# Kernel optimization log

Hardware: AMD Instinct MI355X
Metric: run time of the kernel (lower is better)

Reference implementation:

```python
import math
import jax, jax.numpy as jnp
import numpy as np

N_STEPS = 4
D_ENERGY = 128
FEATURE_DIM = 1024
B, N = 4, 2048


def setup_inputs() -> dict:
    key = jax.random.key(0)
    ks = jax.random.split(key, 5)
    scale = 1.0 / math.sqrt(FEATURE_DIM)
    return {
        "features": jax.random.normal(ks[0], (B, N, FEATURE_DIM), dtype=jnp.float32),
        "W_q": jax.random.normal(ks[1], (FEATURE_DIM, D_ENERGY), dtype=jnp.float32) * scale,
        "W_k": jax.random.normal(ks[2], (FEATURE_DIM, D_ENERGY), dtype=jnp.float32) * scale,
        "charge_w": jax.random.normal(ks[3], (FEATURE_DIM, 1), dtype=jnp.float32) * scale,
        "charge_b": jnp.zeros((1,), dtype=jnp.float32),
        "locality_scale": jnp.float32(1.0),
        "step_size": jnp.float32(0.5),
        "charge_decay": jnp.float32(0.3),
    }


def reference(features, W_q, W_k, charge_w, charge_b, locality_scale, step_size, charge_decay):
    Bn, Nn, _ = features.shape
    # compatibility: [B,N,N]
    Q = jnp.einsum("bnf,fe->bne", features, W_q)
    K = jnp.einsum("bnf,fe->bne", features, W_k)
    compat = jnp.einsum("bqe,bke->bqk", Q, K) / jnp.sqrt(jnp.float32(D_ENERGY))
    # locality bias: locality_scale / max(|i-j|, 1)
    pos = jnp.arange(Nn, dtype=jnp.float32)
    dist = jnp.maximum(jnp.abs(pos[None, :] - pos[:, None]), 1.0)
    locality = locality_scale / dist  # [N,N]
    # initial charge in (0,1): [B,N]
    charge = jax.nn.sigmoid(jnp.einsum("bnf,fo->bno", features, charge_w)[..., 0] + charge_b[0])
    base = compat + locality[None]  # [B,N,N], fixed across steps
    logits = base
    for _ in range(N_STEPS):
        attn = jax.nn.softmax(logits, axis=-1)
        received = attn.sum(axis=-2)  # [B,N] column sums
        charge = charge * (1.0 - charge_decay * jax.nn.sigmoid(received - 1.0))
        energy = -base * charge[..., :, None] * charge[..., None, :]
        logits = logits - step_size * energy
    return jax.nn.softmax(logits, axis=-1)
```

## Files before the change

### kernel.cpp

```cpp
#include <hip/hip_runtime.h>
#include <math.h>

namespace {
constexpr int NB = 4;
constexpr int NN = 2048;
constexpr int FD = 1024;
constexpr int DE = 128;
constexpr int BN = NB * NN;

constexpr size_t PARTQ_OFF = 0;
constexpr size_t PARTK_OFF = 4194304;
constexpr size_t FH_OFF    = 8388608;
constexpr size_t FL_OFF    = 12582912;
constexpr size_t QKHL_OFF  = 16777216;
constexpr size_t C_OFF     = QKHL_OFF + 2097152;
}

typedef __attribute__((ext_vector_type(8))) short bf16x8;
typedef __attribute__((ext_vector_type(4))) float f32x4;
typedef __attribute__((ext_vector_type(4))) _Float16 f16x4;

__device__ __forceinline__ unsigned short bf16_hi(float x) {
    unsigned u = __float_as_uint(x);
    unsigned r = (u + 0x7fffu + ((u >> 16) & 1u)) >> 16;
    return (unsigned short)r;
}
__device__ __forceinline__ float bf16_val(unsigned short h) {
    return __uint_as_float((unsigned)h << 16);
}


__global__ __launch_bounds__(256) void convert_F(
        const float* __restrict__ feat, unsigned short* __restrict__ Fh,
        unsigned short* __restrict__ Fl) {
    const int g = blockIdx.x * 256 + threadIdx.x;
    const int tile = g >> 6, lane = g & 63;
    const int tr = tile >> 5, fc = tile & 31;
    const int row = tr * 16 + (lane & 15);
    const int f0 = fc * 32 + (lane >> 4) * 8;
    const float* src = &feat[(size_t)row * FD + f0];
    ushort4 h0, l0, h1, l1;
    float4 a = *(const float4*)src;
    float4 b = *(const float4*)(src + 4);
    h0.x = bf16_hi(a.x); l0.x = bf16_hi(a.x - bf16_val(h0.x));
    h0.y = bf16_hi(a.y); l0.y = bf16_hi(a.y - bf16_val(h0.y));
    h0.z = bf16_hi(a.z); l0.z = bf16_hi(a.z - bf16_val(h0.z));
    h0.w = bf16_hi(a.w); l0.w = bf16_hi(a.w - bf16_val(h0.w));
    h1.x = bf16_hi(b.x); l1.x = bf16_hi(b.x - bf16_val(h1.x));
    h1.y = bf16_hi(b.y); l1.y = bf16_hi(b.y - bf16_val(h1.y));
    h1.z = bf16_hi(b.z); l1.z = bf16_hi(b.z - bf16_val(h1.z));
    h1.w = bf16_hi(b.w); l1.w = bf16_hi(b.w - bf16_val(h1.w));
    const size_t dst = (size_t)tile * 512 + lane * 8;
    *(ushort4*)&Fh[dst] = h0; *(ushort4*)&Fh[dst + 4] = h1;
    *(ushort4*)&Fl[dst] = l0; *(ushort4*)&Fl[dst + 4] = l1;
}

__global__ __launch_bounds__(256) void convert_W(
        const float* __restrict__ Wq, const float* __restrict__ Wk,
        unsigned short* __restrict__ Wqh, unsigned short* __restrict__ Wql,
        unsigned short* __restrict__ Wkh, unsigned short* __restrict__ Wkl) {
    const int g = blockIdx.x * 256 + threadIdx.x;
    const int tile = g >> 6, lane = g & 63;
    const int ec = tile >> 5, fc = tile & 31;
    const int e = ec * 16 + (lane & 15);
    const int f0 = fc * 32 + (lane >> 4) * 8;
    const float* W = blockIdx.y ? Wk : Wq;
    unsigned short* Th = blockIdx.y ? Wkh : Wqh;
    unsigned short* Tl = blockIdx.y ? Wkl : Wql;
    unsigned short hh[8], ll[8];
    #pragma unroll
    for (int j = 0; j < 8; ++j) {
        float v = W[(size_t)(f0 + j) * DE + e];
        hh[j] = bf16_hi(v); ll[j] = bf16_hi(v - bf16_val(hh[j]));
    }
    const size_t dst = (size_t)tile * 512 + lane * 8;
    *(ushort4*)&Th[dst]     = make_ushort4(hh[0], hh[1], hh[2], hh[3]);
    *(ushort4*)&Th[dst + 4] = make_ushort4(hh[4], hh[5], hh[6], hh[7]);
    *(ushort4*)&Tl[dst]     = make_ushort4(ll[0], ll[1], ll[2], ll[3]);
    *(ushort4*)&Tl[dst + 4] = make_ushort4(ll[4], ll[5], ll[6], ll[7]);
}

__global__ __launch_bounds__(256) void charge_init(
        const float* __restrict__ feat, const float* __restrict__ cw,
        const float* __restrict__ cb, float* __restrict__ c0) {
    const int wave = threadIdx.x >> 6, lane = threadIdx.x & 63;
    const int r = blockIdx.x * 4 + wave;
    const float* fr = feat + (size_t)r * FD;
    float s = 0.f;
    #pragma unroll
    for (int k = 0; k < 16; ++k) { int f = lane + 64 * k; s += fr[f] * cw[f]; }
    for (int off = 32; off > 0; off >>= 1) s += __shfl_xor(s, off);
    if (lane == 0) {
        float x = s + cb[0];
        c0[r] = 1.f / (1.f + __expf(-x));
    }
}

__global__ __launch_bounds__(256) void qk_mfma(
        const unsigned short* __restrict__ Fh, const unsigned short* __restrict__ Fl,
        const unsigned short* __restrict__ Wqh, const unsigned short* __restrict__ Wql,
        const unsigned short* __restrict__ Wkh, const unsigned short* __restrict__ Wkl,
        float* __restrict__ partQ, float* __restrict__ partK) {
    const int tid = threadIdx.x;
    const int w = tid >> 6, lane = tid & 63;
    const int quad = lane >> 4, l16 = lane & 15;
    const int kc = blockIdx.x;
    const int tr0 = blockIdx.y * 4;
    const unsigned short* Bh = (w < 2) ? Wqh : Wkh;
    const unsigned short* Bl = (w < 2) ? Wql : Wkl;
    const int ec0 = (w & 1) * 4;
    float* part = ((w < 2) ? partQ : partK) + (size_t)kc * BN * DE;

    f32x4 acc[4][4];
    #pragma unroll
    for (int a = 0; a < 4; ++a)
        #pragma unroll
        for (int c = 0; c < 4; ++c) acc[a][c] = (f32x4){0.f, 0.f, 0.f, 0.f};

    #pragma unroll 2
    for (int ch = 0; ch < 8; ++ch) {
        const int fc = kc * 8 + ch;
        bf16x8 aH[4], aL[4];
        #pragma unroll
        for (int rt = 0; rt < 4; ++rt) {
            const size_t off = ((size_t)((tr0 + rt) * 32 + fc) * 64 + lane) * 8;
            aH[rt] = *(const bf16x8*)&Fh[off];
            aL[rt] = *(const bf16x8*)&Fl[off];
        }
        #pragma unroll
        for (int ct = 0; ct < 4; ++ct) {
            const size_t off = ((size_t)((ec0 + ct) * 32 + fc) * 64 + lane) * 8;
            bf16x8 bH = *(const bf16x8*)&Bh[off];
            bf16x8 bL = *(const bf16x8*)&Bl[off];
            #pragma unroll
            for (int rt = 0; rt < 4; ++rt) {
                acc[rt][ct] = __builtin_amdgcn_mfma_f32_16x16x32_bf16(aH[rt], bH, acc[rt][ct], 0, 0, 0);
                acc[rt][ct] = __builtin_amdgcn_mfma_f32_16x16x32_bf16(aH[rt], bL, acc[rt][ct], 0, 0, 0);
                acc[rt][ct] = __builtin_amdgcn_mfma_f32_16x16x32_bf16(aL[rt], bH, acc[rt][ct], 0, 0, 0);
            }
        }
    }
    #pragma unroll
    for (int rt = 0; rt < 4; ++rt)
        #pragma unroll
        for (int ct = 0; ct < 4; ++ct)
            #pragma unroll
            for (int reg = 0; reg < 4; ++reg) {
                const int row = (tr0 + rt) * 16 + quad * 4 + reg;
                const int e = (ec0 + ct) * 16 + l16;
                part[(size_t)row * DE + e] = acc[rt][ct][reg];
            }
}

__global__ __launch_bounds__(256) void qk_reduce(
        const float* __restrict__ partQ, const float* __restrict__ partK,
        unsigned short* __restrict__ Qh, unsigned short* __restrict__ Ql,
        unsigned short* __restrict__ Kh, unsigned short* __restrict__ Kl) {
    const size_t i4 = ((size_t)blockIdx.x * 256 + threadIdx.x) * 4;
    float4 q = {0.f, 0.f, 0.f, 0.f}, k = {0.f, 0.f, 0.f, 0.f};
    #pragma unroll
    for (int c = 0; c < 4; ++c) {
        float4 a = *(const float4*)&partQ[(size_t)c * BN * DE + i4];
        float4 b = *(const float4*)&partK[(size_t)c * BN * DE + i4];
        q.x += a.x; q.y += a.y; q.z += a.z; q.w += a.w;
        k.x += b.x; k.y += b.y; k.z += b.z; k.w += b.w;
    }
    const int row = (int)(i4 >> 7);
    const int k0  = (int)(i4 & 127);
    const int kc = k0 >> 5, quad = (k0 >> 3) & 3, j = k0 & 7;
    const int lane = quad * 16 + (row & 15);
    const size_t dst = ((size_t)((row >> 4) * 4 + kc) * 64 + lane) * 8 + j;
    ushort4 h, l;
    h.x = bf16_hi(q.x); l.x = bf16_hi(q.x - bf16_val(h.x));
    h.y = bf16_hi(q.y); l.y = bf16_hi(q.y - bf16_val(h.y));
    h.z = bf16_hi(q.z); l.z = bf16_hi(q.z - bf16_val(h.z));
    h.w = bf16_hi(q.w); l.w = bf16_hi(q.w - bf16_val(h.w));
    *(ushort4*)&Qh[dst] = h; *(ushort4*)&Ql[dst] = l;
    h.x = bf16_hi(k.x); l.x = bf16_hi(k.x - bf16_val(h.x));
    h.y = bf16_hi(k.y); l.y = bf16_hi(k.y - bf16_val(h.y));
    h.z = bf16_hi(k.z); l.z = bf16_hi(k.z - bf16_val(h.z));
    h.w = bf16_hi(k.w); l.w = bf16_hi(k.w - bf16_val(h.w));
    *(ushort4*)&Kh[dst] = h; *(ushort4*)&Kl[dst] = l;
}

__global__ __launch_bounds__(256) void base_mfma(
        const unsigned short* __restrict__ Qh, const unsigned short* __restrict__ Ql,
        const unsigned short* __restrict__ Kh, const unsigned short* __restrict__ Kl,
        const float* __restrict__ d_ls, _Float16* __restrict__ baseH) {
    const int tid = threadIdx.x;
    const int w = tid >> 6, lane = tid & 63;
    const int quad = lane >> 4, l16 = lane & 15;
    const int b = blockIdx.z;
    const int i0 = blockIdx.y * 128, j0 = blockIdx.x * 128;
    const int trA0 = (b * NN + i0) / 16 + w * 2;
    const int trB0 = (b * NN + j0) / 16;

    f32x4 acc[2][8];
    #pragma unroll
    for (int a = 0; a < 2; ++a)
        #pragma unroll
        for (int c = 0; c < 8; ++c) acc[a][c] = (f32x4){0.f, 0.f, 0.f, 0.f};

    #pragma unroll
    for (int kc = 0; kc < 4; ++kc) {
        bf16x8 aH[2], aL[2];
        #pragma unroll
        for (int rt = 0; rt < 2; ++rt) {
            const size_t off = ((size_t)((trA0 + rt) * 4 + kc) * 64 + lane) * 8;
            aH[rt] = *(const bf16x8*)&Qh[off];
            aL[rt] = *(const bf16x8*)&Ql[off];
        }
        #pragma unroll
        for (int ct = 0; ct < 8; ++ct) {
            const size_t off = ((size_t)((trB0 + ct) * 4 + kc) * 64 + lane) * 8;
            bf16x8 bH = *(const bf16x8*)&Kh[off];
            bf16x8 bL = *(const bf16x8*)&Kl[off];
            #pragma unroll
            for (int rt = 0; rt < 2; ++rt) {
                acc[rt][ct] = __builtin_amdgcn_mfma_f32_16x16x32_bf16(aH[rt], bH, acc[rt][ct], 0, 0, 0);
                acc[rt][ct] = __builtin_amdgcn_mfma_f32_16x16x32_bf16(aH[rt], bL, acc[rt][ct], 0, 0, 0);
                acc[rt][ct] = __builtin_amdgcn_mfma_f32_16x16x32_bf16(aL[rt], bH, acc[rt][ct], 0, 0, 0);
            }
        }
    }
    const float ls = d_ls[0];
    const float rs = 0.08838834764831845f;
    #pragma unroll
    for (int rt = 0; rt < 2; ++rt)
        #pragma unroll
        for (int reg = 0; reg < 4; ++reg) {
            const int i = i0 + w * 32 + rt * 16 + quad * 4 + reg;
            _Float16* brow = baseH + ((size_t)b * NN + i) * NN;
            #pragma unroll
            for (int ct = 0; ct < 8; ++ct) {
                const int j = j0 + ct * 16 + l16;
                const float dist = fmaxf(fabsf((float)(i - j)), 1.0f);
                brow[j] = (_Float16)(acc[rt][ct][reg] * rs + ls / dist);
            }
        }
}

template <int T>
__device__ __forceinline__ void row_core(
        const f16x4 (&hv)[8], const float* __restrict__ chg1,
        const float (&ci)[T > 0 ? T : 1], const int lane,
        float (&x)[32], float& inv) {
    float mx = -1e30f;
    #pragma unroll
    for (int k = 0; k < 8; ++k) {
        const int c = k * 256 + lane * 4;
        float m0 = 1.f, m1 = 1.f, m2 = 1.f, m3 = 1.f;
        #pragma unroll
        for (int u = 0; u < T; ++u) {
            const float4 cj = *(const float4*)&chg1[(size_t)u * BN + c];
            m0 += ci[u] * cj.x; m1 += ci[u] * cj.y;
            m2 += ci[u] * cj.z; m3 += ci[u] * cj.w;
        }
        x[k * 4 + 0] = (float)hv[k][0] * m0;
        x[k * 4 + 1] = (float)hv[k][1] * m1;
        x[k * 4 + 2] = (float)hv[k][2] * m2;
        x[k * 4 + 3] = (float)hv[k][3] * m3;
        mx = fmaxf(mx, fmaxf(fmaxf(x[k * 4], x[k * 4 + 1]),
                             fmaxf(x[k * 4 + 2], x[k * 4 + 3])));
    }
    #pragma unroll
    for (int off = 32; off > 0; off >>= 1) mx = fmaxf(mx, __shfl_xor(mx, off));
    float se = 0.f;
    #pragma unroll
    for (int q = 0; q < 32; ++q) { x[q] = __expf(x[q] - mx); se += x[q]; }
    #pragma unroll
    for (int off = 32; off > 0; off >>= 1) se += __shfl_xor(se, off);
    inv = 1.f / se;
}

template <int T, bool WO>
__global__ __launch_bounds__(256) void step_pass(
        const _Float16* __restrict__ base, const float* __restrict__ charge,
        const float* __restrict__ d_ss, float* __restrict__ P,
        float* __restrict__ out) {
    constexpr int CS_W = WO ? 1 : 4;
    constexpr int CS_N = WO ? 1 : NN;
    __shared__ float colsum[CS_W][CS_N];
    const int tid = threadIdx.x;
    const int w = tid >> 6, lane = tid & 63;
    const int blk = blockIdx.x;
    const int b = blk >> 8;
    const int r0 = (blk & 255) * 8;
    const float ss = d_ss[0];
    const size_t cb = (size_t)b << 11;
    const size_t ri0 = cb + r0 + w * 2;
    const _Float16* row0 = base + ri0 * NN;
    const _Float16* row1 = row0 + NN;
    const float* chg1 = charge + (size_t)BN + cb;

    f16x4 hv0[8], hv1[8];
    #pragma unroll
    for (int k = 0; k < 8; ++k) {
        const int c = k * 256 + lane * 4;
        hv0[k] = *(const f16x4*)&row0[c];
        hv1[k] = *(const f16x4*)&row1[c];
    }
    float ci0[T > 0 ? T : 1], ci1[T > 0 ? T : 1];
    #pragma unroll
    for (int u = 0; u < T; ++u) {
        ci0[u] = charge[(size_t)(u + 1) * BN + ri0] * ss;
        ci1[u] = charge[(size_t)(u + 1) * BN + ri0 + 1] * ss;
    }

    float col_acc[32];
    if (!WO) {
        #pragma unroll
        for (int q = 0; q < 32; ++q) col_acc[q] = 0.f;
    }

    float x[32]; float inv;
    row_core<T>(hv0, chg1, ci0, lane, x, inv);
    if (WO) {
        #pragma unroll
        for (int k = 0; k < 8; ++k) {
            const int c = k * 256 + lane * 4;
            float4 o = {x[k * 4 + 0] * inv, x[k * 4 + 1] * inv,
                        x[k * 4 + 2] * inv, x[k * 4 + 3] * inv};
            *(float4*)&out[ri0 * NN + c] = o;
        }
    } else {
        #pragma unroll
        for (int q = 0; q < 32; ++q) col_acc[q] += x[q] * inv;
    }
    row_core<T>(hv1, chg1, ci1, lane, x, inv);
    if (WO) {
        #pragma unroll
        for (int k = 0; k < 8; ++k) {
            const int c = k * 256 + lane * 4;
            float4 o = {x[k * 4 + 0] * inv, x[k * 4 + 1] * inv,
                        x[k * 4 + 2] * inv, x[k * 4 + 3] * inv};
            *(float4*)&out[(ri0 + 1) * NN + c] = o;
        }
    } else {
        #pragma unroll
        for (int q = 0; q < 32; ++q) col_acc[q] += x[q] * inv;
    }

    if (!WO) {
        #pragma unroll
        for (int k = 0; k < 8; ++k)
            *(float4*)&colsum[w][k * 256 + lane * 4] = *(float4*)&col_acc[k * 4];
        __syncthreads();
        float* prow = P + (size_t)blk * NN;
        #pragma unroll
        for (int k = 0; k < 8; ++k) {
            const int c = tid + 256 * k;
            prow[c] = colsum[0][c] + colsum[1][c] + colsum[2][c] + colsum[3][c];
        }
    }
}

__global__ __launch_bounds__(256) void charge_reduce(
        const float* __restrict__ P, const float* __restrict__ d_decay,
        const float* __restrict__ c_prev, float* __restrict__ c_next) {
    const int b = blockIdx.x >> 3;
    const int col = ((blockIdx.x & 7) << 8) + threadIdx.x;
    const float* p = P + ((size_t)b * 256) * NN + col;
    float s = 0.f;
    #pragma unroll 8
    for (int r = 0; r < 256; ++r) s += p[(size_t)r * NN];
    const int gi = (b << 11) + col;
    const float sg = 1.f / (1.f + __expf(1.f - s));
    c_next[gi] = c_prev[gi] * (1.f - d_decay[0] * sg);
}

extern "C" void kernel_launch(void* const* d_in, const int* in_sizes, int n_in,
                              void* d_out, int out_size, void* d_ws, size_t ws_size,
                              hipStream_t stream) {
    const float* feat  = (const float*)d_in[0];
    const float* Wq    = (const float*)d_in[1];
    const float* Wk    = (const float*)d_in[2];
    const float* cw    = (const float*)d_in[3];
    const float* cb    = (const float*)d_in[4];
    const float* ls    = (const float*)d_in[5];
    const float* ssp   = (const float*)d_in[6];
    const float* decay = (const float*)d_in[7];

    float* ws   = (float*)d_ws;
    float* partQ = ws + PARTQ_OFF;
    float* partK = ws + PARTK_OFF;
    unsigned short* Fh = (unsigned short*)(ws + FH_OFF);
    unsigned short* Fl = (unsigned short*)(ws + FL_OFF);
    unsigned short* qkhl = (unsigned short*)(ws + QKHL_OFF);
    unsigned short* Qh = qkhl;
    unsigned short* Ql = qkhl + (size_t)BN * DE;
    unsigned short* Kh = qkhl + (size_t)2 * BN * DE;
    unsigned short* Kl = qkhl + (size_t)3 * BN * DE;
    unsigned short* Wqh = qkhl;
    unsigned short* Wql = qkhl + (size_t)DE * FD;
    unsigned short* Wkh = qkhl + (size_t)2 * DE * FD;
    unsigned short* Wkl = qkhl + (size_t)3 * DE * FD;
    float* charge = ws + C_OFF;
    _Float16* baseH = (_Float16*)(ws + PARTQ_OFF);
    float* P      = ws + FH_OFF;
    float* out    = (float*)d_out;

    convert_F<<<BN * FD / 8 / 256, 256, 0, stream>>>(feat, Fh, Fl);
    convert_W<<<dim3(64, 2), 256, 0, stream>>>(Wq, Wk, Wqh, Wql, Wkh, Wkl);
    charge_init<<<BN / 4, 256, 0, stream>>>(feat, cw, cb, charge);
    qk_mfma<<<dim3(4, BN / 64), 256, 0, stream>>>(Fh, Fl, Wqh, Wql, Wkh, Wkl, partQ, partK);
    qk_reduce<<<BN * DE / 4 / 256, 256, 0, stream>>>(partQ, partK, Qh, Ql, Kh, Kl);
    base_mfma<<<dim3(NN / 128, NN / 128, NB), 256, 0, stream>>>(Qh, Ql, Kh, Kl, ls, baseH);

    step_pass<0, false><<<1024, 256, 0, stream>>>(baseH, charge, ssp, P, nullptr);
    charge_reduce<<<32, 256, 0, stream>>>(P, decay, charge, charge + (size_t)BN);
    step_pass<1, false><<<1024, 256, 0, stream>>>(baseH, charge, ssp, P, nullptr);
    charge_reduce<<<32, 256, 0, stream>>>(P, decay, charge + (size_t)BN, charge + (size_t)2 * BN);
    step_pass<2, false><<<1024, 256, 0, stream>>>(baseH, charge, ssp, P, nullptr);
    charge_reduce<<<32, 256, 0, stream>>>(P, decay, charge + (size_t)2 * BN, charge + (size_t)3 * BN);
    step_pass<3, false><<<1024, 256, 0, stream>>>(baseH, charge, ssp, P, nullptr);
    charge_reduce<<<32, 256, 0, stream>>>(P, decay, charge + (size_t)3 * BN, charge + (size_t)4 * BN);
    step_pass<4, true><<<1024, 256, 0, stream>>>(baseH, charge, ssp, nullptr, out);
}
```

Before: 276.4 us.

## Fuse prep kernels, drop split-K QK reduce, stage charges in LDS for softmax steps

Merges the feature/weight conversion and charge-init kernels into one launch, and replaces the split-K QK projection plus reduction with a single kernel that writes hi/lo bf16 Q/K via LDS. The step passes now cache charge vectors in shared memory, use wider f16 loads, skip the softmax max subtraction, and reduce column sums in two stages. This cuts launches, partial-sum traffic and redundant global loads, at the cost of fewer blocks in the projection and reliance on bounded logits to avoid exp overflow.

```diff
diff --git a/kernel.cpp b/kernel.cpp
--- a/kernel.cpp
+++ b/kernel.cpp
@@ -8,8 +8,7 @@
 constexpr int DE = 128;
 constexpr int BN = NB * NN;
 
-constexpr size_t PARTQ_OFF = 0;
-constexpr size_t PARTK_OFF = 4194304;
+constexpr size_t WSW_OFF   = 0;
 constexpr size_t FH_OFF    = 8388608;
 constexpr size_t FL_OFF    = 12582912;
 constexpr size_t QKHL_OFF  = 16777216;
@@ -18,7 +17,7 @@
 
 typedef __attribute__((ext_vector_type(8))) short bf16x8;
 typedef __attribute__((ext_vector_type(4))) float f32x4;
-typedef __attribute__((ext_vector_type(4))) _Float16 f16x4;
+typedef __attribute__((ext_vector_type(8))) _Float16 f16x8;
 
 __device__ __forceinline__ unsigned short bf16_hi(float x) {
     unsigned u = __float_as_uint(x);
@@ -30,157 +29,132 @@
 }
 
 
-__global__ __launch_bounds__(256) void convert_F(
-        const float* __restrict__ feat, unsigned short* __restrict__ Fh,
-        unsigned short* __restrict__ Fl) {
-    const int g = blockIdx.x * 256 + threadIdx.x;
-    const int tile = g >> 6, lane = g & 63;
-    const int tr = tile >> 5, fc = tile & 31;
-    const int row = tr * 16 + (lane & 15);
-    const int f0 = fc * 32 + (lane >> 4) * 8;
-    const float* src = &feat[(size_t)row * FD + f0];
-    ushort4 h0, l0, h1, l1;
-    float4 a = *(const float4*)src;
-    float4 b = *(const float4*)(src + 4);
-    h0.x = bf16_hi(a.x); l0.x = bf16_hi(a.x - bf16_val(h0.x));
-    h0.y = bf16_hi(a.y); l0.y = bf16_hi(a.y - bf16_val(h0.y));
-    h0.z = bf16_hi(a.z); l0.z = bf16_hi(a.z - bf16_val(h0.z));
-    h0.w = bf16_hi(a.w); l0.w = bf16_hi(a.w - bf16_val(h0.w));
-    h1.x = bf16_hi(b.x); l1.x = bf16_hi(b.x - bf16_val(h1.x));
-    h1.y = bf16_hi(b.y); l1.y = bf16_hi(b.y - bf16_val(h1.y));
-    h1.z = bf16_hi(b.z); l1.z = bf16_hi(b.z - bf16_val(h1.z));
-    h1.w = bf16_hi(b.w); l1.w = bf16_hi(b.w - bf16_val(h1.w));
-    const size_t dst = (size_t)tile * 512 + lane * 8;
-    *(ushort4*)&Fh[dst] = h0; *(ushort4*)&Fh[dst + 4] = h1;
-    *(ushort4*)&Fl[dst] = l0; *(ushort4*)&Fl[dst + 4] = l1;
-}
-
-__global__ __launch_bounds__(256) void convert_W(
-        const float* __restrict__ Wq, const float* __restrict__ Wk,
+__global__ __launch_bounds__(256) void prep(
+        const float* __restrict__ feat, const float* __restrict__ Wq,
+        const float* __restrict__ Wk, const float* __restrict__ cw,
+        const float* __restrict__ cbias,
+        unsigned short* __restrict__ Fh, unsigned short* __restrict__ Fl,
         unsigned short* __restrict__ Wqh, unsigned short* __restrict__ Wql,
-        unsigned short* __restrict__ Wkh, unsigned short* __restrict__ Wkl) {
-    const int g = blockIdx.x * 256 + threadIdx.x;
-    const int tile = g >> 6, lane = g & 63;
-    const int ec = tile >> 5, fc = tile & 31;
-    const int e = ec * 16 + (lane & 15);
-    const int f0 = fc * 32 + (lane >> 4) * 8;
-    const float* W = blockIdx.y ? Wk : Wq;
-    unsigned short* Th = blockIdx.y ? Wkh : Wqh;
-    unsigned short* Tl = blockIdx.y ? Wkl : Wql;
-    unsigned short hh[8], ll[8];
-    #pragma unroll
-    for (int j = 0; j < 8; ++j) {
-        float v = W[(size_t)(f0 + j) * DE + e];
-        hh[j] = bf16_hi(v); ll[j] = bf16_hi(v - bf16_val(hh[j]));
-    }
-    const size_t dst = (size_t)tile * 512 + lane * 8;
-    *(ushort4*)&Th[dst]     = make_ushort4(hh[0], hh[1], hh[2], hh[3]);
-    *(ushort4*)&Th[dst + 4] = make_ushort4(hh[4], hh[5], hh[6], hh[7]);
-    *(ushort4*)&Tl[dst]     = make_ushort4(ll[0], ll[1], ll[2], ll[3]);
-    *(ushort4*)&Tl[dst + 4] = make_ushort4(ll[4], ll[5], ll[6], ll[7]);
-}
-
-__global__ __launch_bounds__(256) void charge_init(
-        const float* __restrict__ feat, const float* __restrict__ cw,
-        const float* __restrict__ cb, float* __restrict__ c0) {
-    const int wave = threadIdx.x >> 6, lane = threadIdx.x & 63;
-    const int r = blockIdx.x * 4 + wave;
-    const float* fr = feat + (size_t)r * FD;
-    float s = 0.f;
-    #pragma unroll
-    for (int k = 0; k < 16; ++k) { int f = lane + 64 * k; s += fr[f] * cw[f]; }
-    for (int off = 32; off > 0; off >>= 1) s += __shfl_xor(s, off);
-    if (lane == 0) {
-        float x = s + cb[0];
-        c0[r] = 1.f / (1.f + __expf(-x));
-    }
-}
-
-__global__ __launch_bounds__(256) void qk_mfma(
+        unsigned short* __restrict__ Wkh, unsigned short* __restrict__ Wkl,
+        float* __restrict__ c0) {
+    const int bid = blockIdx.x;
+    const int tid = threadIdx.x;
+    if (bid < 4096) {
+        const int g = bid * 256 + tid;
+        const int tile = g >> 6, lane = g & 63;
+        const int tr = tile >> 5, fc = tile & 31;
+        const int row = tr * 16 + (lane & 15);
+        const int f0 = fc * 32 + (lane >> 4) * 8;
+        const float* src = &feat[(size_t)row * FD + f0];
+        ushort4 h0, l0, h1, l1;
+        float4 a = *(const float4*)src;
+        float4 b = *(const float4*)(src + 4);
+        h0.x = bf16_hi(a.x); l0.x = bf16_hi(a.x - bf16_val(h0.x));
+        h0.y = bf16_hi(a.y); l0.y = bf16_hi(a.y - bf16_val(h0.y));
+        h0.z = bf16_hi(a.z); l0.z = bf16_hi(a.z - bf16_val(h0.z));
+        h0.w = bf16_hi(a.w); l0.w = bf16_hi(a.w - bf16_val(h0.w));
+        h1.x = bf16_hi(b.x); l1.x = bf16_hi(b.x - bf16_val(h1.x));
+        h1.y = bf16_hi(b.y); l1.y = bf16_hi(b.y - bf16_val(h1.y));
+        h1.z = bf16_hi(b.z); l1.z = bf16_hi(b.z - bf16_val(h1.z));
+        h1.w = bf16_hi(b.w); l1.w = bf16_hi(b.w - bf16_val(h1.w));
+        const size_t dst = (size_t)tile * 512 + lane * 8;
+        *(ushort4*)&Fh[dst] = h0; *(ushort4*)&Fh[dst + 4] = h1;
+        *(ushort4*)&Fl[dst] = l0; *(ushort4*)&Fl[dst + 4] = l1;
+    } else if (bid < 4224) {
+        const int wbid = bid - 4096;
+        const int mat = wbid >> 6;
+        const int g = (wbid & 63) * 256 + tid;
+        const int tile = g >> 6, lane = g & 63;
+        const int ec = tile >> 5, fc = tile & 31;
+        const int e = ec * 16 + (lane & 15);
+        const int f0 = fc * 32 + (lane >> 4) * 8;
+        const float* W = mat ? Wk : Wq;
+        unsigned short* Th = mat ? Wkh : Wqh;
+        unsigned short* Tl = mat ? Wkl : Wql;
+        unsigned short hh[8], ll[8];
+        #pragma unroll
+        for (int j = 0; j < 8; ++j) {
+            float v = W[(size_t)(f0 + j) * DE + e];
+            hh[j] = bf16_hi(v); ll[j] = bf16_hi(v - bf16_val(hh[j]));
+        }
+        const size_t dst = (size_t)tile * 512 + lane * 8;
+        *(ushort4*)&Th[dst]     = make_ushort4(hh[0], hh[1], hh[2], hh[3]);
+        *(ushort4*)&Th[dst + 4] = make_ushort4(hh[4], hh[5], hh[6], hh[7]);
+        *(ushort4*)&Tl[dst]     = make_ushort4(ll[0], ll[1], ll[2], ll[3]);
+        *(ushort4*)&Tl[dst + 4] = make_ushort4(ll[4], ll[5], ll[6], ll[7]);
+    } else {
+        const int wave = tid >> 6, lane = tid & 63;
+        const int r = (bid - 4224) * 4 + wave;
+        const float* fr = feat + (size_t)r * FD;
+        float s = 0.f;
+        #pragma unroll
+        for (int k = 0; k < 16; ++k) { int f = lane + 64 * k; s += fr[f] * cw[f]; }
+        for (int off = 32; off > 0; off >>= 1) s += __shfl_xor(s, off);
+        if (lane == 0) {
+            float x = s + cbias[0];
+            c0[r] = 1.f / (1.f + __expf(-x));
+        }
+    }
+}
+
+__global__ __launch_bounds__(256) void qk_proj(
         const unsigned short* __restrict__ Fh, const unsigned short* __restrict__ Fl,
         const unsigned short* __restrict__ Wqh, const unsigned short* __restrict__ Wql,
         const unsigned short* __restrict__ Wkh, const unsigned short* __restrict__ Wkl,
-        float* __restrict__ partQ, float* __restrict__ partK) {
+        unsigned short* __restrict__ Qh, unsigned short* __restrict__ Ql,
+        unsigned short* __restrict__ Kh, unsigned short* __restrict__ Kl) {
+    __shared__ unsigned short lds[8192];
     const int tid = threadIdx.x;
     const int w = tid >> 6, lane = tid & 63;
     const int quad = lane >> 4, l16 = lane & 15;
-    const int kc = blockIdx.x;
-    const int tr0 = blockIdx.y * 4;
-    const unsigned short* Bh = (w < 2) ? Wqh : Wkh;
-    const unsigned short* Bl = (w < 2) ? Wql : Wkl;
-    const int ec0 = (w & 1) * 4;
-    float* part = ((w < 2) ? partQ : partK) + (size_t)kc * BN * DE;
-
-    f32x4 acc[4][4];
-    #pragma unroll
-    for (int a = 0; a < 4; ++a)
-        #pragma unroll
-        for (int c = 0; c < 4; ++c) acc[a][c] = (f32x4){0.f, 0.f, 0.f, 0.f};
-
-    #pragma unroll 2
-    for (int ch = 0; ch < 8; ++ch) {
-        const int fc = kc * 8 + ch;
-        bf16x8 aH[4], aL[4];
-        #pragma unroll
-        for (int rt = 0; rt < 4; ++rt) {
-            const size_t off = ((size_t)((tr0 + rt) * 32 + fc) * 64 + lane) * 8;
-            aH[rt] = *(const bf16x8*)&Fh[off];
-            aL[rt] = *(const bf16x8*)&Fl[off];
-        }
+    const int blk = blockIdx.x;
+    const int mat = w >> 1, ec0 = (w & 1) * 4;
+    const unsigned short* Bh = mat ? Wkh : Wqh;
+    const unsigned short* Bl = mat ? Wkl : Wql;
+
+    f32x4 acc[4];
+    #pragma unroll
+    for (int c = 0; c < 4; ++c) acc[c] = (f32x4){0.f, 0.f, 0.f, 0.f};
+
+    for (int fc = 0; fc < 32; ++fc) {
+        const size_t aoff = ((size_t)(blk * 32 + fc) * 64 + lane) * 8;
+        bf16x8 aH = *(const bf16x8*)&Fh[aoff];
+        bf16x8 aL = *(const bf16x8*)&Fl[aoff];
         #pragma unroll
         for (int ct = 0; ct < 4; ++ct) {
-            const size_t off = ((size_t)((ec0 + ct) * 32 + fc) * 64 + lane) * 8;
-            bf16x8 bH = *(const bf16x8*)&Bh[off];
-            bf16x8 bL = *(const bf16x8*)&Bl[off];
-            #pragma unroll
-            for (int rt = 0; rt < 4; ++rt) {
-                acc[rt][ct] = __builtin_amdgcn_mfma_f32_16x16x32_bf16(aH[rt], bH, acc[rt][ct], 0, 0, 0);
-                acc[rt][ct] = __builtin_amdgcn_mfma_f32_16x16x32_bf16(aH[rt], bL, acc[rt][ct], 0, 0, 0);
-                acc[rt][ct] = __builtin_amdgcn_mfma_f32_16x16x32_bf16(aL[rt], bH, acc[rt][ct], 0, 0, 0);
-            }
-        }
-    }
-    #pragma unroll
-    for (int rt = 0; rt < 4; ++rt)
-        #pragma unroll
-        for (int ct = 0; ct < 4; ++ct)
-            #pragma unroll
-            for (int reg = 0; reg < 4; ++reg) {
-                const int row = (tr0 + rt) * 16 + quad * 4 + reg;
-                const int e = (ec0 + ct) * 16 + l16;
-                part[(size_t)row * DE + e] = acc[rt][ct][reg];
-            }
-}
-
-__global__ __launch_bounds__(256) void qk_reduce(
-        const float* __restrict__ partQ, const float* __restrict__ partK,
-        unsigned short* __restrict__ Qh, unsigned short* __restrict__ Ql,
-        unsigned short* __restrict__ Kh, unsigned short* __restrict__ Kl) {
-    const size_t i4 = ((size_t)blockIdx.x * 256 + threadIdx.x) * 4;
-    float4 q = {0.f, 0.f, 0.f, 0.f}, k = {0.f, 0.f, 0.f, 0.f};
-    #pragma unroll
-    for (int c = 0; c < 4; ++c) {
-        float4 a = *(const float4*)&partQ[(size_t)c * BN * DE + i4];
-        float4 b = *(const float4*)&partK[(size_t)c * BN * DE + i4];
-        q.x += a.x; q.y += a.y; q.z += a.z; q.w += a.w;
-        k.x += b.x; k.y += b.y; k.z += b.z; k.w += b.w;
-    }
-    const int row = (int)(i4 >> 7);
-    const int k0  = (int)(i4 & 127);
-    const int kc = k0 >> 5, quad = (k0 >> 3) & 3, j = k0 & 7;
-    const int lane = quad * 16 + (row & 15);
-    const size_t dst = ((size_t)((row >> 4) * 4 + kc) * 64 + lane) * 8 + j;
-    ushort4 h, l;
-    h.x = bf16_hi(q.x); l.x = bf16_hi(q.x - bf16_val(h.x));
-    h.y = bf16_hi(q.y); l.y = bf16_hi(q.y - bf16_val(h.y));
-    h.z = bf16_hi(q.z); l.z = bf16_hi(q.z - bf16_val(h.z));
-    h.w = bf16_hi(q.w); l.w = bf16_hi(q.w - bf16_val(h.w));
-    *(ushort4*)&Qh[dst] = h; *(ushort4*)&Ql[dst] = l;
-    h.x = bf16_hi(k.x); l.x = bf16_hi(k.x - bf16_val(h.x));
-    h.y = bf16_hi(k.y); l.y = bf16_hi(k.y - bf16_val(h.y));
-    h.z = bf16_hi(k.z); l.z = bf16_hi(k.z - bf16_val(h.z));
-    h.w = bf16_hi(k.w); l.w = bf16_hi(k.w - bf16_val(h.w));
-    *(ushort4*)&Kh[dst] = h; *(ushort4*)&Kl[dst] = l;
+            const size_t boff = ((size_t)((ec0 + ct) * 32 + fc) * 64 + lane) * 8;
+            bf16x8 bH = *(const bf16x8*)&Bh[boff];
+            bf16x8 bL = *(const bf16x8*)&Bl[boff];
+            acc[ct] = __builtin_amdgcn_mfma_f32_16x16x32_bf16(aH, bH, acc[ct], 0, 0, 0);
+            acc[ct] = __builtin_amdgcn_mfma_f32_16x16x32_bf16(aH, bL, acc[ct], 0, 0, 0);
+            acc[ct] = __builtin_amdgcn_mfma_f32_16x16x32_bf16(aL, bH, acc[ct], 0, 0, 0);
+        }
+    }
+    #pragma unroll
+    for (int ct = 0; ct < 4; ++ct) {
+        const int e = (ec0 + ct) * 16 + l16;
+        const int kc = e >> 5, q2 = (e >> 3) & 3, j2 = e & 7;
+        #pragma unroll
+        for (int reg = 0; reg < 4; ++reg) {
+            const int rl = quad * 4 + reg;
+            const float v = acc[ct][reg];
+            const unsigned short h = bf16_hi(v);
+            const unsigned short l = bf16_hi(v - bf16_val(h));
+            const int idx = (kc * 64 + q2 * 16 + rl) * 8 + j2;
+            lds[(mat * 2 + 0) * 2048 + idx] = h;
+            lds[(mat * 2 + 1) * 2048 + idx] = l;
+        }
+    }
+    __syncthreads();
+    const size_t gbase = (size_t)blk * 2048;
+    unsigned short* const dsts[4] = {Qh, Ql, Kh, Kl};
+    #pragma unroll
+    for (int ch = 0; ch < 4; ++ch) {
+        const int o = ch * 2048 + tid * 8;
+        unsigned short* dst = dsts[ch] + gbase + tid * 8;
+        *(ushort4*)&dst[0] = *(const ushort4*)&lds[o];
+        *(ushort4*)&dst[4] = *(const ushort4*)&lds[o + 4];
+    }
 }
 
 __global__ __launch_bounds__(256) void base_mfma(
@@ -240,45 +214,14 @@
         }
 }
 
-template <int T>
-__device__ __forceinline__ void row_core(
-        const f16x4 (&hv)[8], const float* __restrict__ chg1,
-        const float (&ci)[T > 0 ? T : 1], const int lane,
-        float (&x)[32], float& inv) {
-    float mx = -1e30f;
-    #pragma unroll
-    for (int k = 0; k < 8; ++k) {
-        const int c = k * 256 + lane * 4;
-        float m0 = 1.f, m1 = 1.f, m2 = 1.f, m3 = 1.f;
-        #pragma unroll
-        for (int u = 0; u < T; ++u) {
-            const float4 cj = *(const float4*)&chg1[(size_t)u * BN + c];
-            m0 += ci[u] * cj.x; m1 += ci[u] * cj.y;
-            m2 += ci[u] * cj.z; m3 += ci[u] * cj.w;
-        }
-        x[k * 4 + 0] = (float)hv[k][0] * m0;
-        x[k * 4 + 1] = (float)hv[k][1] * m1;
-        x[k * 4 + 2] = (float)hv[k][2] * m2;
-        x[k * 4 + 3] = (float)hv[k][3] * m3;
-        mx = fmaxf(mx, fmaxf(fmaxf(x[k * 4], x[k * 4 + 1]),
-                             fmaxf(x[k * 4 + 2], x[k * 4 + 3])));
-    }
-    #pragma unroll
-    for (int off = 32; off > 0; off >>= 1) mx = fmaxf(mx, __shfl_xor(mx, off));
-    float se = 0.f;
-    #pragma unroll
-    for (int q = 0; q < 32; ++q) { x[q] = __expf(x[q] - mx); se += x[q]; }
-    #pragma unroll
-    for (int off = 32; off > 0; off >>= 1) se += __shfl_xor(se, off);
-    inv = 1.f / se;
-}
-
 template <int T, bool WO>
 __global__ __launch_bounds__(256) void step_pass(
         const _Float16* __restrict__ base, const float* __restrict__ charge,
         const float* __restrict__ d_ss, float* __restrict__ P,
         float* __restrict__ out) {
-    constexpr int CS_W = WO ? 1 : 4;
+    constexpr int TS = T > 0 ? T : 1;
+    __shared__ float cjs[TS][NN];
+    constexpr int CS_W = WO ? 1 : 2;
     constexpr int CS_N = WO ? 1 : NN;
     __shared__ float colsum[CS_W][CS_N];
     const int tid = threadIdx.x;
@@ -289,23 +232,20 @@
     const float ss = d_ss[0];
     const size_t cb = (size_t)b << 11;
     const size_t ri0 = cb + r0 + w * 2;
-    const _Float16* row0 = base + ri0 * NN;
-    const _Float16* row1 = row0 + NN;
-    const float* chg1 = charge + (size_t)BN + cb;
-
-    f16x4 hv0[8], hv1[8];
-    #pragma unroll
-    for (int k = 0; k < 8; ++k) {
-        const int c = k * 256 + lane * 4;
-        hv0[k] = *(const f16x4*)&row0[c];
-        hv1[k] = *(const f16x4*)&row1[c];
-    }
-    float ci0[T > 0 ? T : 1], ci1[T > 0 ? T : 1];
+
     #pragma unroll
     for (int u = 0; u < T; ++u) {
-        ci0[u] = charge[(size_t)(u + 1) * BN + ri0] * ss;
-        ci1[u] = charge[(size_t)(u + 1) * BN + ri0 + 1] * ss;
-    }
+        const float* src = &charge[(size_t)(u + 1) * BN + cb + tid * 8];
+        *(float4*)&cjs[u][tid * 8]     = *(const float4*)&src[0];
+        *(float4*)&cjs[u][tid * 8 + 4] = *(const float4*)&src[4];
+    }
+    float ci[2][TS];
+    #pragma unroll
+    for (int u = 0; u < T; ++u) {
+        ci[0][u] = charge[(size_t)(u + 1) * BN + ri0] * ss;
+        ci[1][u] = charge[(size_t)(u + 1) * BN + ri0 + 1] * ss;
+    }
+    if (T > 0) __syncthreads();
 
     float col_acc[32];
     if (!WO) {
@@ -313,44 +253,88 @@
         for (int q = 0; q < 32; ++q) col_acc[q] = 0.f;
     }
 
-    float x[32]; float inv;
-    row_core<T>(hv0, chg1, ci0, lane, x, inv);
-    if (WO) {
-        #pragma unroll
-        for (int k = 0; k < 8; ++k) {
-            const int c = k * 256 + lane * 4;
-            float4 o = {x[k * 4 + 0] * inv, x[k * 4 + 1] * inv,
-                        x[k * 4 + 2] * inv, x[k * 4 + 3] * inv};
-            *(float4*)&out[ri0 * NN + c] = o;
-        }
-    } else {
-        #pragma unroll
-        for (int q = 0; q < 32; ++q) col_acc[q] += x[q] * inv;
-    }
-    row_core<T>(hv1, chg1, ci1, lane, x, inv);
-    if (WO) {
-        #pragma unroll
-        for (int k = 0; k < 8; ++k) {
-            const int c = k * 256 + lane * 4;
-            float4 o = {x[k * 4 + 0] * inv, x[k * 4 + 1] * inv,
-                        x[k * 4 + 2] * inv, x[k * 4 + 3] * inv};
-            *(float4*)&out[(ri0 + 1) * NN + c] = o;
-        }
-    } else {
-        #pragma unroll
-        for (int q = 0; q < 32; ++q) col_acc[q] += x[q] * inv;
+    #pragma unroll
+    for (int r = 0; r < 2; ++r) {
+        const _Float16* row = base + (ri0 + r) * NN;
+        f16x8 hv[4];
+        #pragma unroll
+        for (int k = 0; k < 4; ++k)
+            hv[k] = *(const f16x8*)&row[k * 512 + lane * 8];
+        float x[32];
+        float se = 0.f;
+        #pragma unroll
+        for (int k = 0; k < 4; ++k) {
+            const int c = k * 512 + lane * 8;
+            float m[8];
+            #pragma unroll
+            for (int j = 0; j < 8; ++j) m[j] = 1.f;
+            #pragma unroll
+            for (int u = 0; u < T; ++u) {
+                const float4 a0 = *(const float4*)&cjs[u][c];
+                const float4 a1 = *(const float4*)&cjs[u][c + 4];
+                const float cu = ci[r][u];
+                m[0] += cu * a0.x; m[1] += cu * a0.y;
+                m[2] += cu * a0.z; m[3] += cu * a0.w;
+                m[4] += cu * a1.x; m[5] += cu * a1.y;
+                m[6] += cu * a1.z; m[7] += cu * a1.w;
+            }
+            #pragma unroll
+            for (int j = 0; j < 8; ++j) {
+                const float v = __expf((float)hv[k][j] * m[j]);
+                x[k * 8 + j] = v;
+                se += v;
+            }
+        }
+        #pragma unroll
+        for (int off = 32; off > 0; off >>= 1) se += __shfl_xor(se, off);
+        const float inv = 1.f / se;
+        if (WO) {
+            #pragma unroll
+            for (int k = 0; k < 4; ++k) {
+                const int c = k * 512 + lane * 8;
+                float4 o0 = {x[k * 8 + 0] * inv, x[k * 8 + 1] * inv,
+                             x[k * 8 + 2] * inv, x[k * 8 + 3] * inv};
+                float4 o1 = {x[k * 8 + 4] * inv, x[k * 8 + 5] * inv,
+                             x[k * 8 + 6] * inv, x[k * 8 + 7] * inv};
+                *(float4*)&out[(ri0 + r) * NN + c]     = o0;
+                *(float4*)&out[(ri0 + r) * NN + c + 4] = o1;
+            }
+        } else {
+            #pragma unroll
+            for (int q = 0; q < 32; ++q) col_acc[q] += x[q] * inv;
+        }
     }
 
     if (!WO) {
-        #pragma unroll
-        for (int k = 0; k < 8; ++k)
-            *(float4*)&colsum[w][k * 256 + lane * 4] = *(float4*)&col_acc[k * 4];
+        if (w < 2) {
+            #pragma unroll
+            for (int k = 0; k < 4; ++k) {
+                const int c = k * 512 + lane * 8;
+                *(float4*)&colsum[w][c]     = *(float4*)&col_acc[k * 8];
+                *(float4*)&colsum[w][c + 4] = *(float4*)&col_acc[k * 8 + 4];
+            }
+        }
+        __syncthreads();
+        if (w >= 2) {
+            #pragma unroll
+            for (int k = 0; k < 4; ++k) {
+                const int c = k * 512 + lane * 8;
+                float4 s0 = *(const float4*)&colsum[w - 2][c];
+                float4 s1 = *(const float4*)&colsum[w - 2][c + 4];
+                s0.x += col_acc[k * 8 + 0]; s0.y += col_acc[k * 8 + 1];
+                s0.z += col_acc[k * 8 + 2]; s0.w += col_acc[k * 8 + 3];
+                s1.x += col_acc[k * 8 + 4]; s1.y += col_acc[k * 8 + 5];
+                s1.z += col_acc[k * 8 + 6]; s1.w += col_acc[k * 8 + 7];
+                *(float4*)&colsum[w - 2][c]     = s0;
+                *(float4*)&colsum[w - 2][c + 4] = s1;
+            }
+        }
         __syncthreads();
         float* prow = P + (size_t)blk * NN;
         #pragma unroll
         for (int k = 0; k < 8; ++k) {
             const int c = tid + 256 * k;
-            prow[c] = colsum[0][c] + colsum[1][c] + colsum[2][c] + colsum[3][c];
+            prow[c] = colsum[0][c] + colsum[1][c];
         }
     }
 }
@@ -382,8 +366,6 @@
     const float* decay = (const float*)d_in[7];
 
     float* ws   = (float*)d_ws;
-    float* partQ = ws + PARTQ_OFF;
-    float* partK = ws + PARTK_OFF;
     unsigned short* Fh = (unsigned short*)(ws + FH_OFF);
     unsigned short* Fl = (unsigned short*)(ws + FL_OFF);
     unsigned short* qkhl = (unsigned short*)(ws + QKHL_OFF);
@@ -391,21 +373,21 @@
     unsigned short* Ql = qkhl + (size_t)BN * DE;
     unsigned short* Kh = qkhl + (size_t)2 * BN * DE;
     unsigned short* Kl = qkhl + (size_t)3 * BN * DE;
-    unsigned short* Wqh = qkhl;
-    unsigned short* Wql = qkhl + (size_t)DE * FD;
-    unsigned short* Wkh = qkhl + (size_t)2 * DE * FD;
-    unsigned short* Wkl = qkhl + (size_t)3 * DE * FD;
+    unsigned short* Wqh = (unsigned short*)(ws + WSW_OFF);
+    unsigned short* Wql = Wqh + (size_t)DE * FD;
+    unsigned short* Wkh = Wqh + (size_t)2 * DE * FD;
+    unsigned short* Wkl = Wqh + (size_t)3 * DE * FD;
     float* charge = ws + C_OFF;
-    _Float16* baseH = (_Float16*)(ws + PARTQ_OFF);
+    _Float16* baseH = (_Float16*)(ws + WSW_OFF);
     float* P      = ws + FH_OFF;
     float* out    = (float*)d_out;
 
-    convert_F<<<BN * FD / 8 / 256, 256, 0, stream>>>(feat, Fh, Fl);
-    convert_W<<<dim3(64, 2), 256, 0, stream>>>(Wq, Wk, Wqh, Wql, Wkh, Wkl);
-    charge_init<<<BN / 4, 256, 0, stream>>>(feat, cw, cb, charge);
-    qk_mfma<<<dim3(4, BN / 64), 256, 0, stream>>>(Fh, Fl, Wqh, Wql, Wkh, Wkl, partQ, partK);
-    qk_reduce<<<BN * DE / 4 / 256, 256, 0, stream>>>(partQ, partK, Qh, Ql, Kh, Kl);
-    base_mfma<<<dim3(NN / 128, NN / 128, NB), 256, 0, stream>>>(Qh, Ql, Kh, Kl, ls, baseH);
+    prep<<<6272, 256, 0, stream>>>(feat, Wq, Wk, cw, cb,
+                                   Fh, Fl, Wqh, Wql, Wkh, Wkl, charge);
+    qk_proj<<<512, 256, 0, stream>>>(Fh, Fl, Wqh, Wql, Wkh, Wkl,
+                                     Qh, Ql, Kh, Kl);
+    base_mfma<<<dim3(NN / 128, NN / 128, NB), 256, 0, stream>>>(
+        Qh, Ql, Kh, Kl, ls, baseH);
 
     step_pass<0, false><<<1024, 256, 0, stream>>>(baseH, charge, ssp, P, nullptr);
     charge_reduce<<<32, 256, 0, stream>>>(P, decay, charge, charge + (size_t)BN);
```

New measurement: 315.3 us. +14.1%, slower.
